# Kernel tuning notes

Hardware: AMD Instinct MI355X
Metric: run time of the kernel (lower is better)

The kernel has to match this reference:

```python
import jax, jax.numpy as jnp
import numpy as np

N, DIM = 8192, 128

def setup_inputs() -> dict:
    key = jax.random.key(0)
    k1, k2, k3 = jax.random.split(key, 3)
    latent = jax.random.normal(k1, (N, DIM), dtype=jnp.float32)
    coords = jax.random.normal(k2, (N, 3), dtype=jnp.float32) * 5.0  # protein-scale spread
    alpha = jax.random.uniform(k3, (N,), dtype=jnp.float32)  # valid exponent range
    return {"latent": latent, "coords": coords, "alpha": alpha}

def _pairwise_dist(coords):
    # Euclidean cdist without materializing [N,N,3]
    sq = jnp.sum(coords * coords, axis=-1)  # [N]
    d2 = sq[:, None] + sq[None, :] - 2.0 * (coords @ coords.T)  # [N,N]
    return jnp.sqrt(jnp.maximum(d2, 1e-12))

def reference(latent, coords, alpha):
    D = _pairwise_dist(coords) + 1e-6  # [N,N]
    a = 0.5 * (alpha[:, None] + alpha[None, :])  # [N,N]
    # torch.no_grad() block -> stop_gradient on the clamped distance base
    D_safe = jax.lax.stop_gradient(jnp.clip(D, 1e-6, None))
    K = jnp.clip(D_safe ** (-a), 1e-8, 1000.0) * jnp.exp(-D / 12.0)
    K = jnp.clip(K, 0.0, 1000.0)
    n = K.shape[0]
    K = K * (1.0 - jnp.eye(n, dtype=K.dtype))  # fill_diagonal_(0)
    K = K / (jnp.sum(K, axis=-1, keepdims=True) + 1e-8)  # row-normalize
    out = K @ latent  # [N,DIM] aggregation
    return out, K
```

## Files before the change

kernel.cpp:

```cpp
#include <hip/hip_runtime.h>
#include <hip/hip_bf16.h>

constexpr int kN = 8192;
constexpr int kD = 128;
constexpr int BM = 32;
constexpr int BK = 64;
constexpr int JSPLIT = 8;
constexpr int LDB = 72;
constexpr int TB = 64;
constexpr int NB = kN / TB;

typedef __bf16 v8bf __attribute__((ext_vector_type(8)));
typedef float  v4f  __attribute__((ext_vector_type(4)));

__device__ __forceinline__ void gload16(const void* g, void* l) {
    __builtin_amdgcn_global_load_lds(
        (const __attribute__((address_space(1))) void*)g,
        (__attribute__((address_space(3))) void*)l, 16, 0, 0);
}

__device__ __forceinline__ float kraw_f(float4 ci, float sqi, float4 cj, float sqj) {
    float d2 = sqi + sqj - 2.0f * (ci.x * cj.x + ci.y * cj.y + ci.z * cj.z);
    d2 = fmaxf(d2, 1e-12f);
    float Dd = __builtin_amdgcn_sqrtf(d2);
    float a = 0.5f * (ci.w + cj.w);
    float t = a * (-0.5f * __builtin_amdgcn_logf(d2));
    t = fminf(fmaxf(t, -26.575424759098897f), 9.965784284662087f);
    float K = __builtin_amdgcn_exp2f(fmaf(Dd, -0.12022458674074695f, t));
    return fminf(K, 1000.0f);
}

__global__ void pack_k(const float* __restrict__ coords, const float* __restrict__ alpha,
                       float4* __restrict__ c4, float* __restrict__ rsum) {
    int j = blockIdx.x * 256 + threadIdx.x;
    if (j < kN) {
        c4[j] = make_float4(coords[3 * j], coords[3 * j + 1], coords[3 * j + 2], alpha[j]);
        rsum[j] = 0.0f;
    }
}

__global__ void transpose_k(const float* __restrict__ latent, __bf16* __restrict__ latT,
                            float* __restrict__ outp) {
    __shared__ float tile[32][33];
    int t = threadIdx.x;
    int tx = t & 31, ty = t >> 5;
    int j0 = blockIdx.x * 32, d0 = blockIdx.y * 32;
    #pragma unroll
    for (int i = 0; i < 32; i += 8)
        tile[ty + i][tx] = latent[(size_t)(j0 + ty + i) * kD + d0 + tx];

    {
        size_t base = (((size_t)blockIdx.x * 4 + blockIdx.y) * 256 + t) * 4;
        v4f z = {0.f, 0.f, 0.f, 0.f};
        *reinterpret_cast<v4f*>(outp + base) = z;
    }
    __syncthreads();
    #pragma unroll
    for (int i = 0; i < 32; i += 8)
        latT[(size_t)(d0 + ty + i) * kN + j0 + tx] = (__bf16)tile[tx][ty + i];
}

__global__ __launch_bounds__(256) void rowsum_sym_k(const float4* __restrict__ c4,
                                                    float* __restrict__ rsum) {
    __shared__ float4 rc4[TB];
    __shared__ float  rsq[TB];
    __shared__ float  rowbuf[TB][TB + 1];

    int L = blockIdx.x;
    int bi = (int)((2 * NB + 1 - sqrtf((float)((2 * NB + 1) * (2 * NB + 1) - 8 * L))) * 0.5f);
    #pragma unroll
    for (int f = 0; f < 2; ++f) {
        int s0 = bi * NB - bi * (bi - 1) / 2;
        int s1 = (bi + 1) * NB - (bi + 1) * bi / 2;
        if (L >= s1) ++bi;
        else if (L < s0) --bi;
    }
    int sbi = bi * NB - bi * (bi - 1) / 2;
    int bj = bi + (L - sbi);
    bool diag = (bi == bj);

    const int t = threadIdx.x;
    const int l = t & 63;
    const int w = t >> 6;

    if (t < TB) {
        float4 ci = c4[bi * TB + t];
        rc4[t] = ci;
        rsq[t] = ci.x * ci.x + ci.y * ci.y + ci.z * ci.z;
    }
    __syncthreads();

    float4 cj = c4[bj * TB + l];
    float sqj = cj.x * cj.x + cj.y * cj.y + cj.z * cj.z;

    float colacc = 0.f;
    #pragma unroll
    for (int rr = 0; rr < 16; ++rr) {
        int r = w * 16 + rr;
        float k = kraw_f(rc4[r], rsq[r], cj, sqj);
        if (diag && r == l) k = 0.f;
        colacc += k;
        rowbuf[r][l] = k;
    }
    __syncthreads();

    {
        int r = t >> 2, q = t & 3;
        float p = 0.f;
        #pragma unroll
        for (int m = 0; m < 16; ++m) p += rowbuf[r][q * 16 + m];
        p += __shfl_xor(p, 1, 64);
        p += __shfl_xor(p, 2, 64);
        if (q == 0) atomicAdd(&rsum[bi * TB + r], p);
    }
    if (!diag) atomicAdd(&rsum[bj * TB + l], colacc);
}

__global__ __launch_bounds__(256, 2) void main_k(
    const float4* __restrict__ c4, const float* __restrict__ rsum,
    const __bf16* __restrict__ latT, float* __restrict__ outp, float* __restrict__ Kout) {

    __shared__ __bf16 Alds[BM][LDB];
    __shared__ __bf16 Blin[kD * BK];
    __shared__ float4 c4row[BM];
    __shared__ float  sqrow[BM];
    __shared__ float  invrow[BM];

    const int t = threadIdx.x;
    const int i0 = blockIdx.x * BM;
    const int jstrip = blockIdx.y * (kN / JSPLIT);

    if (t < BM) {
        float4 ci = c4[i0 + t];
        c4row[t] = ci;
        sqrow[t] = ci.x * ci.x + ci.y * ci.y + ci.z * ci.z;
        invrow[t] = 1.0f / (rsum[i0 + t] + 1e-8f);
    }
    __syncthreads();

    const int lane = t & 63;
    const int wave = t >> 6;

    const int c2 = t & 31;
    const int rb = (t >> 5) * 4;

    float4 rc[4]; float rs[4], rv[4];
    #pragma unroll
    for (int rr = 0; rr < 4; ++rr) {
        rc[rr] = c4row[rb + rr];
        rs[rr] = sqrow[rb + rr];
        rv[rr] = invrow[rb + rr];
    }

    const int arow = lane & 15;
    const int koff = (lane >> 4) * 8;
    const int dbase = wave * 32;
    const int bswz = ((dbase + arow) & 7) << 4;

    const int srow = t >> 3;
    const int scolb = ((t & 7) ^ (srow & 7)) << 4;

    v4f acc[2][2];
    #pragma unroll
    for (int rt = 0; rt < 2; ++rt)
        #pragma unroll
        for (int dt = 0; dt < 2; ++dt) acc[rt][dt] = (v4f){0.f, 0.f, 0.f, 0.f};

    for (int cb = 0; cb < kN / JSPLIT / BK; ++cb) {
        const int j0 = jstrip + cb * BK;

        #pragma unroll
        for (int it = 0; it < 4; ++it) {
            int row = it * 32 + srow;
            const char* src = (const char*)latT + ((size_t)row * kN + j0) * 2 + scolb;
            char* dst = (char*)Blin + it * 4096 + t * 16;
            gload16(src, dst);
        }

        const int gjA = j0 + 2 * c2, gjB = gjA + 1;
        const float4 cjA = c4[gjA];
        const float4 cjB = c4[gjB];
        const float sqA = cjA.x * cjA.x + cjA.y * cjA.y + cjA.z * cjA.z;
        const float sqB = cjB.x * cjB.x + cjB.y * cjB.y + cjB.z * cjB.z;
        #pragma unroll
        for (int rr = 0; rr < 4; ++rr) {
            int r = rb + rr, gi = i0 + r;
            float kA = (gi == gjA) ? 0.0f : kraw_f(rc[rr], rs[rr], cjA, sqA);
            float kB = (gi == gjB) ? 0.0f : kraw_f(rc[rr], rs[rr], cjB, sqB);
            float knA = kA * rv[rr];
            float knB = kB * rv[rr];
            float2 st = {knA, knB};
            *reinterpret_cast<float2*>(Kout + (size_t)gi * kN + gjA) = st;
            __bf16 hA = (__bf16)knA, hB = (__bf16)knB;
            unsigned pk = ((unsigned)*(unsigned short*)&hB << 16) | *(unsigned short*)&hA;
            *reinterpret_cast<unsigned*>(&Alds[r][2 * c2]) = pk;
        }
        __syncthreads();

        #pragma unroll
        for (int kk = 0; kk < 2; ++kk) {
            v8bf a0 = *reinterpret_cast<const v8bf*>(&Alds[arow][kk * 32 + koff]);
            v8bf a1 = *reinterpret_cast<const v8bf*>(&Alds[16 + arow][kk * 32 + koff]);
            const int bc = kk * 64 + koff * 2;
            const char* bp0 = (const char*)Blin + (dbase + arow) * 128 + (bc ^ bswz);
            const char* bp1 = (const char*)Blin + (dbase + 16 + arow) * 128 + (bc ^ bswz);
            v8bf b0 = *reinterpret_cast<const v8bf*>(bp0);
            v8bf b1 = *reinterpret_cast<const v8bf*>(bp1);
            acc[0][0] = __builtin_amdgcn_mfma_f32_16x16x32_bf16(a0, b0, acc[0][0], 0, 0, 0);
            acc[0][1] = __builtin_amdgcn_mfma_f32_16x16x32_bf16(a0, b1, acc[0][1], 0, 0, 0);
            acc[1][0] = __builtin_amdgcn_mfma_f32_16x16x32_bf16(a1, b0, acc[1][0], 0, 0, 0);
            acc[1][1] = __builtin_amdgcn_mfma_f32_16x16x32_bf16(a1, b1, acc[1][1], 0, 0, 0);
        }
        __syncthreads();
    }

    const int row = (lane >> 4) * 4;
    const int col0 = wave * 32 + (lane & 15);
    #pragma unroll
    for (int rt = 0; rt < 2; ++rt)
        #pragma unroll
        for (int dt = 0; dt < 2; ++dt)
            #pragma unroll
            for (int q = 0; q < 4; ++q)
                atomicAdd(&outp[(size_t)(i0 + rt * 16 + row + q) * kD + col0 + dt * 16],
                          acc[rt][dt][q]);
}

extern "C" void kernel_launch(void* const* d_in, const int* in_sizes, int n_in,
                              void* d_out, int out_size, void* d_ws, size_t ws_size,
                              hipStream_t stream) {
    const float* latent = (const float*)d_in[0];
    const float* coords = (const float*)d_in[1];
    const float* alpha  = (const float*)d_in[2];

    float* outp = (float*)d_out;
    float* Kout = (float*)d_out + (size_t)kN * kD;

    char* ws = (char*)d_ws;
    __bf16* latT = (__bf16*)ws;
    float4* c4   = (float4*)(ws + 2u * 1024 * 1024);
    float*  rsum = (float*)(ws + 2u * 1024 * 1024 + 128 * 1024);

    pack_k<<<dim3(kN / 256), dim3(256), 0, stream>>>(coords, alpha, c4, rsum);
    transpose_k<<<dim3(kN / 32, kD / 32), dim3(256), 0, stream>>>(latent, latT, outp);
    rowsum_sym_k<<<dim3(NB * (NB + 1) / 2), dim3(256), 0, stream>>>(c4, rsum);
    main_k<<<dim3(kN / BM, JSPLIT), dim3(256), 0, stream>>>(c4, rsum, latT, outp, Kout);
}
```

Measured before the change: 117.1 us.

## Pre-pack latent into MFMA fragment layout and load B directly from global

Replaces the plain transpose with a prep kernel that writes latent as bf16 in the exact per-lane MFMA B-fragment order. The main kernel then loads B fragments straight from global or L2 into registers instead of staging through LDS with global_load_lds and swizzled reads. This removes LDS traffic and the B staging from the main loop. In exchange, each wave issues its own global loads, and the same B data is read redundantly by many blocks, which relies on cache hits and exposes global latency.

```diff
diff --git a/kernel.cpp b/kernel.cpp
--- a/kernel.cpp
+++ b/kernel.cpp
@@ -12,12 +12,6 @@
 
 typedef __bf16 v8bf __attribute__((ext_vector_type(8)));
 typedef float  v4f  __attribute__((ext_vector_type(4)));
-
-__device__ __forceinline__ void gload16(const void* g, void* l) {
-    __builtin_amdgcn_global_load_lds(
-        (const __attribute__((address_space(1))) void*)g,
-        (__attribute__((address_space(3))) void*)l, 16, 0, 0);
-}
 
 __device__ __forceinline__ float kraw_f(float4 ci, float sqi, float4 cj, float sqj) {
     float d2 = sqi + sqj - 2.0f * (ci.x * cj.x + ci.y * cj.y + ci.z * cj.z);
@@ -39,25 +33,47 @@
     }
 }
 
-__global__ void transpose_k(const float* __restrict__ latent, __bf16* __restrict__ latT,
-                            float* __restrict__ outp) {
-    __shared__ float tile[32][33];
-    int t = threadIdx.x;
-    int tx = t & 31, ty = t >> 5;
-    int j0 = blockIdx.x * 32, d0 = blockIdx.y * 32;
-    #pragma unroll
-    for (int i = 0; i < 32; i += 8)
-        tile[ty + i][tx] = latent[(size_t)(j0 + ty + i) * kD + d0 + tx];
+__global__ __launch_bounds__(256) void fragprep_k(const float* __restrict__ latent,
+                                                  __bf16* __restrict__ latTf,
+                                                  float* __restrict__ outp) {
+    __shared__ float ltile[32][132];
+    const int jw = blockIdx.x;
+    const int t = threadIdx.x;
+
+    #pragma unroll
+    for (int it = 0; it < 4; ++it) {
+        int idx = it * 256 + t;
+        int row = idx >> 5;
+        int col = (idx & 31) * 4;
+        float4 v = *reinterpret_cast<const float4*>(
+            latent + (size_t)(jw * 32 + row) * kD + col);
+        *reinterpret_cast<float4*>(&ltile[row][col]) = v;
+    }
 
     {
-        size_t base = (((size_t)blockIdx.x * 4 + blockIdx.y) * 256 + t) * 4;
+        size_t base = ((size_t)jw * 256 + t) * 16;
         v4f z = {0.f, 0.f, 0.f, 0.f};
-        *reinterpret_cast<v4f*>(outp + base) = z;
-    }
-    __syncthreads();
-    #pragma unroll
-    for (int i = 0; i < 32; i += 8)
-        latT[(size_t)(d0 + ty + i) * kN + j0 + tx] = (__bf16)tile[tx][ty + i];
+        #pragma unroll
+        for (int e = 0; e < 4; ++e)
+            *reinterpret_cast<v4f*>(outp + base + e * 4) = z;
+    }
+    __syncthreads();
+
+    #pragma unroll
+    for (int ss = 0; ss < 2; ++ss) {
+        int s = ss * 256 + t;
+        int d = s >> 6, l = s & 63;
+        int jr = (l >> 4) * 8, dim = d * 16 + (l & 15);
+        unsigned w[4];
+        #pragma unroll
+        for (int e2 = 0; e2 < 4; ++e2) {
+            __bf16 lo = (__bf16)ltile[jr + 2 * e2][dim];
+            __bf16 hi = (__bf16)ltile[jr + 2 * e2 + 1][dim];
+            w[e2] = ((unsigned)*(unsigned short*)&hi << 16) | *(unsigned short*)&lo;
+        }
+        uint4 out = {w[0], w[1], w[2], w[3]};
+        *reinterpret_cast<uint4*>((char*)latTf + (((size_t)jw * 8 + d) * 64 + l) * 16) = out;
+    }
 }
 
 __global__ __launch_bounds__(256) void rowsum_sym_k(const float4* __restrict__ c4,
@@ -118,10 +134,9 @@
 
 __global__ __launch_bounds__(256, 2) void main_k(
     const float4* __restrict__ c4, const float* __restrict__ rsum,
-    const __bf16* __restrict__ latT, float* __restrict__ outp, float* __restrict__ Kout) {
+    const __bf16* __restrict__ latTf, float* __restrict__ outp, float* __restrict__ Kout) {
 
     __shared__ __bf16 Alds[BM][LDB];
-    __shared__ __bf16 Blin[kD * BK];
     __shared__ float4 c4row[BM];
     __shared__ float  sqrow[BM];
     __shared__ float  invrow[BM];
@@ -154,11 +169,7 @@
 
     const int arow = lane & 15;
     const int koff = (lane >> 4) * 8;
-    const int dbase = wave * 32;
-    const int bswz = ((dbase + arow) & 7) << 4;
-
-    const int srow = t >> 3;
-    const int scolb = ((t & 7) ^ (srow & 7)) << 4;
+    const char* bfb = (const char*)latTf + (size_t)lane * 16;
 
     v4f acc[2][2];
     #pragma unroll
@@ -168,14 +179,6 @@
 
     for (int cb = 0; cb < kN / JSPLIT / BK; ++cb) {
         const int j0 = jstrip + cb * BK;
-
-        #pragma unroll
-        for (int it = 0; it < 4; ++it) {
-            int row = it * 32 + srow;
-            const char* src = (const char*)latT + ((size_t)row * kN + j0) * 2 + scolb;
-            char* dst = (char*)Blin + it * 4096 + t * 16;
-            gload16(src, dst);
-        }
 
         const int gjA = j0 + 2 * c2, gjB = gjA + 1;
         const float4 cjA = c4[gjA];
@@ -199,13 +202,11 @@
 
         #pragma unroll
         for (int kk = 0; kk < 2; ++kk) {
+            const size_t jw = (size_t)(j0 >> 5) + kk;
             v8bf a0 = *reinterpret_cast<const v8bf*>(&Alds[arow][kk * 32 + koff]);
             v8bf a1 = *reinterpret_cast<const v8bf*>(&Alds[16 + arow][kk * 32 + koff]);
-            const int bc = kk * 64 + koff * 2;
-            const char* bp0 = (const char*)Blin + (dbase + arow) * 128 + (bc ^ bswz);
-            const char* bp1 = (const char*)Blin + (dbase + 16 + arow) * 128 + (bc ^ bswz);
-            v8bf b0 = *reinterpret_cast<const v8bf*>(bp0);
-            v8bf b1 = *reinterpret_cast<const v8bf*>(bp1);
+            v8bf b0 = *reinterpret_cast<const v8bf*>(bfb + (jw * 8 + wave * 2)     * 1024);
+            v8bf b1 = *reinterpret_cast<const v8bf*>(bfb + (jw * 8 + wave * 2 + 1) * 1024);
             acc[0][0] = __builtin_amdgcn_mfma_f32_16x16x32_bf16(a0, b0, acc[0][0], 0, 0, 0);
             acc[0][1] = __builtin_amdgcn_mfma_f32_16x16x32_bf16(a0, b1, acc[0][1], 0, 0, 0);
             acc[1][0] = __builtin_amdgcn_mfma_f32_16x16x32_bf16(a1, b0, acc[1][0], 0, 0, 0);
@@ -237,12 +238,12 @@
     float* Kout = (float*)d_out + (size_t)kN * kD;
 
     char* ws = (char*)d_ws;
-    __bf16* latT = (__bf16*)ws;
-    float4* c4   = (float4*)(ws + 2u * 1024 * 1024);
-    float*  rsum = (float*)(ws + 2u * 1024 * 1024 + 128 * 1024);
+    __bf16* latTf = (__bf16*)ws;
+    float4* c4    = (float4*)(ws + 2u * 1024 * 1024);
+    float*  rsum  = (float*)(ws + 2u * 1024 * 1024 + 128 * 1024);
 
     pack_k<<<dim3(kN / 256), dim3(256), 0, stream>>>(coords, alpha, c4, rsum);
-    transpose_k<<<dim3(kN / 32, kD / 32), dim3(256), 0, stream>>>(latent, latT, outp);
+    fragprep_k<<<dim3(kN / 32), dim3(256), 0, stream>>>(latent, latTf, outp);
     rowsum_sym_k<<<dim3(NB * (NB + 1) / 2), dim3(256), 0, stream>>>(c4, rsum);
-    main_k<<<dim3(kN / BM, JSPLIT), dim3(256), 0, stream>>>(c4, rsum, latT, outp, Kout);
-}
+    main_k<<<dim3(kN / BM, JSPLIT), dim3(256), 0, stream>>>(c4, rsum, latTf, outp, Kout);
+}
```

New measurement: 118.5 us. No clear change (+1.2%).
